# Kernel tuning notes

Hardware: AMD Instinct MI355X
Metric: run time of the kernel (lower is better)

Reference implementation:

```python
import jax, jax.numpy as jnp
import numpy as np

N_NODES = 50000
N_EDGES = 640000
D = 128  # input = hidden = output channels (must match for this module's forward to type-check)


def gcn_conv(x, W, b, src, dst, n):
    """PyG GCNConv: out = D^{-1/2} (A + I) D^{-1/2} (x @ W) + b.
    src = edge_index[0] (source/message sender), dst = edge_index[1] (target/aggregation index).
    """
    h = x @ W  # [n, d_out]
    loop = jnp.arange(n)
    s = jnp.concatenate([src, loop])  # add self-loops
    d = jnp.concatenate([dst, loop])
    deg = jax.ops.segment_sum(jnp.ones(s.shape[0], dtype=h.dtype), d, num_segments=n)
    dis = jax.lax.rsqrt(deg)  # deg >= 1 thanks to self-loops
    norm = dis[s] * dis[d]  # [E + n]
    msg = h[s] * norm[:, None]  # gather + scale (largest intermediate)
    return jax.ops.segment_sum(msg, d, num_segments=n) + b


def setup_inputs() -> dict:
    key = jax.random.key(0)
    ks = jax.random.split(key, 9)
    x = jax.random.normal(ks[0], (N_NODES, D), dtype=jnp.float32)
    edge_index_normal = jax.random.randint(ks[1], (2, N_EDGES), 0, N_NODES, dtype=jnp.int64 if jax.config.jax_enable_x64 else jnp.int32)
    edge_index_role = jax.random.randint(ks[2], (2, N_EDGES), 0, N_NODES, dtype=jnp.int64 if jax.config.jax_enable_x64 else jnp.int32)
    s = 1.0 / np.sqrt(D)
    W_role = jax.random.uniform(ks[3], (D, D), jnp.float32, -s, s)
    b_role = jnp.zeros((D,), jnp.float32)
    W2 = jax.random.uniform(ks[4], (D, D), jnp.float32, -s, s)
    b2 = jnp.zeros((D,), jnp.float32)
    W1 = jax.random.uniform(ks[5], (D, D), jnp.float32, -s, s)
    b1 = jnp.zeros((D,), jnp.float32)
    return {"x": x, "W_role": W_role, "b_role": b_role, "W2": W2, "b2": b2,
            "W1": W1, "b1": b1,
            "edge_index_normal": edge_index_normal, "edge_index_role": edge_index_role}


def reference(x, W_role, b_role, W2, b2, W1, b1, edge_index_normal, edge_index_role):
    n = x.shape[0]
    # conv_role on the role graph, then conv2 and conv1 on the normal graph.
    h = jax.nn.relu(gcn_conv(x, W_role, b_role, edge_index_role[0], edge_index_role[1], n))
    # dropout(p=0.5) is identity in eval mode
    h = jax.nn.relu(gcn_conv(h, W2, b2, edge_index_normal[0], edge_index_normal[1], n))
    out = gcn_conv(h, W1, b1, edge_index_normal[0], edge_index_normal[1], n)
    return out
```

## Files before the change

kernel.cpp:

```cpp
#include <hip/hip_runtime.h>
#include <hip/hip_fp16.h>

#define D 128
#define CHUNK 8192
#define BSH 7
#define BNODES 128
#define MAXNB 512
#define CAP 6144

__global__ __launch_bounds__(256) void p1_hist(const int* __restrict__ dst_n,
                                               const int* __restrict__ dst_r,
                                               int En, int Er,
                                               int* __restrict__ base2,
                                               int NB, int NC, int L) {
    int g = blockIdx.x / NC, c = blockIdx.x % NC;
    const int* dst = g ? dst_r : dst_n;
    int E = g ? Er : En;
    __shared__ int hist[MAXNB];
    for (int i = threadIdx.x; i < NB; i += 256) hist[i] = 0;
    __syncthreads();
    int e0 = c * CHUNK, e1 = min(e0 + CHUNK, E);
    for (int e = e0 + threadIdx.x; e < e1; e += 256)
        atomicAdd(&hist[dst[e] >> BSH], 1);
    __syncthreads();
    for (int b = threadIdx.x; b < NB; b += 256)
        base2[g * L + b * NC + c] = hist[b];
}

__global__ __launch_bounds__(1024) void scan_pass1(const int* __restrict__ data,
                                                   int* __restrict__ bsum2, int L, int nb) {
    int g = blockIdx.x / nb, b = blockIdx.x % nb;
    int i = b * 1024 + threadIdx.x;
    int v = (i < L) ? data[g * L + i] : 0;
    #pragma unroll
    for (int off = 32; off; off >>= 1) v += __shfl_down(v, off, 64);
    __shared__ int wsum[16];
    int lane = threadIdx.x & 63, wid = threadIdx.x >> 6;
    if (lane == 0) wsum[wid] = v;
    __syncthreads();
    if (threadIdx.x == 0) {
        int s = 0;
        for (int w = 0; w < 16; ++w) s += wsum[w];
        bsum2[g * 64 + b] = s;
    }
}

__global__ __launch_bounds__(128) void scan_pass2(int* __restrict__ bsum2, int nb) {
    int wid = threadIdx.x >> 6, lane = threadIdx.x & 63;
    int v = (lane < nb) ? bsum2[wid * 64 + lane] : 0;
    int incl = v;
    #pragma unroll
    for (int off = 1; off < 64; off <<= 1) {
        int t = __shfl_up(incl, off, 64);
        if (lane >= off) incl += t;
    }
    if (lane < nb) bsum2[wid * 64 + lane] = incl - v;
}

__global__ __launch_bounds__(1024) void scan_pass3(int* __restrict__ data,
                                                   const int* __restrict__ bsum2,
                                                   int L, int nb) {
    int g = blockIdx.x / nb, b = blockIdx.x % nb;
    int i = b * 1024 + threadIdx.x;
    int v = (i < L) ? data[g * L + i] : 0;
    int lane = threadIdx.x & 63, wid = threadIdx.x >> 6;
    int incl = v;
    #pragma unroll
    for (int off = 1; off < 64; off <<= 1) {
        int t = __shfl_up(incl, off, 64);
        if (lane >= off) incl += t;
    }
    __shared__ int wsum[16];
    if (lane == 63) wsum[wid] = incl;
    __syncthreads();
    if (threadIdx.x == 0) {
        int s = 0;
        for (int w = 0; w < 16; ++w) { int t = wsum[w]; wsum[w] = s; s += t; }
    }
    __syncthreads();
    if (i < L) data[g * L + i] = incl - v + wsum[wid] + bsum2[g * 64 + b];
}

__global__ __launch_bounds__(256) void p2_scatter(const int* __restrict__ src_n,
                                                  const int* __restrict__ dst_n,
                                                  const int* __restrict__ src_r,
                                                  const int* __restrict__ dst_r,
                                                  int En, int Er,
                                                  const int* __restrict__ base2,
                                                  unsigned int* __restrict__ part_n,
                                                  unsigned int* __restrict__ part_r,
                                                  int NB, int NC, int L) {
    int g = blockIdx.x / NC, c = blockIdx.x % NC;
    const int* src = g ? src_r : src_n;
    const int* dst = g ? dst_r : dst_n;
    unsigned int* part = g ? part_r : part_n;
    int E = g ? Er : En;
    __shared__ int cur[MAXNB];
    for (int b = threadIdx.x; b < NB; b += 256)
        cur[b] = base2[g * L + b * NC + c];
    __syncthreads();
    int e0 = c * CHUNK, e1 = min(e0 + CHUNK, E);
    for (int e = e0 + threadIdx.x; e < e1; e += 256) {
        int d = dst[e];
        int pos = atomicAdd(&cur[d >> BSH], 1);
        part[pos] = ((unsigned)d << 16) | (unsigned)src[e];
    }
}

__global__ __launch_bounds__(256) void p3_csr(const unsigned int* __restrict__ part_n,
                                              const unsigned int* __restrict__ part_r,
                                              const int* __restrict__ base2,
                                              int* __restrict__ rs2,
                                              float* __restrict__ dis2,
                                              unsigned short* __restrict__ csr_n,
                                              unsigned short* __restrict__ csr_r,
                                              int n, int NB, int NC, int L, int En, int Er) {
    int g = blockIdx.x / NB, b = blockIdx.x % NB;
    const unsigned int* part = g ? part_r : part_n;
    unsigned short* csr = g ? csr_r : csr_n;
    int E = g ? Er : En;
    __shared__ int deg[BNODES];
    __shared__ int cur[BNODES];
    __shared__ unsigned short buf[CAP];
    __shared__ int w0tot;
    int t = threadIdx.x;
    if (t < BNODES) deg[t] = 0;
    __syncthreads();
    int bstart = base2[g * L + b * NC];
    int bend = (b + 1 < NB) ? base2[g * L + (b + 1) * NC] : E;
    int sz = bend - bstart;
    for (int e = bstart + t; e < bend; e += 256)
        atomicAdd(&deg[(part[e] >> 16) & (BNODES - 1)], 1);
    __syncthreads();
    int incl = 0, v = 0;
    if (t < BNODES) {
        int lane = t & 63;
        v = deg[t];
        incl = v;
        #pragma unroll
        for (int off = 1; off < 64; off <<= 1) {
            int tt = __shfl_up(incl, off, 64);
            if (lane >= off) incl += tt;
        }
        if (t == 63) w0tot = incl;
    }
    __syncthreads();
    if (t < BNODES) {
        int excl = incl - v + ((t >= 64) ? w0tot : 0);
        cur[t] = excl;
        int idx = b * BNODES + t;
        if (idx < n) {
            rs2[g * (n + 1) + idx] = bstart + excl;
            dis2[g * n + idx] = rsqrtf((float)(deg[t] + 1));
        }
    }
    if (b == NB - 1 && t == 255) rs2[g * (n + 1) + n] = E;
    __syncthreads();
    if (sz <= CAP) {
        for (int e = bstart + t; e < bend; e += 256) {
            unsigned int p = part[e];
            int pos = atomicAdd(&cur[(p >> 16) & (BNODES - 1)], 1);
            buf[pos] = (unsigned short)(p & 0xffffu);
        }
        __syncthreads();
        for (int i = t; i < sz; i += 256) csr[bstart + i] = buf[i];
    } else {
        for (int e = bstart + t; e < bend; e += 256) {
            unsigned int p = part[e];
            int pos = atomicAdd(&cur[(p >> 16) & (BNODES - 1)], 1);
            csr[bstart + pos] = (unsigned short)(p & 0xffffu);
        }
    }
}


__global__ __launch_bounds__(256) void gemm_scale(const float* __restrict__ X,
                                                  const float* __restrict__ W,
                                                  const float* __restrict__ dis,
                                                  __half* __restrict__ Y, int n) {
    __shared__ float sX[128 * D];
    int t = threadIdx.x;
    int rg = t >> 4;
    int cg = (t & 15) << 3;
    int rb = blockIdx.x * 128;
    int rows = min(128, n - rb);

    float4* sX4 = (float4*)sX;
    for (int i = t; i < rows * 32; i += 256)
        sX4[i] = ((const float4*)X)[(size_t)rb * 32 + i];
    __syncthreads();

    float acc[8][8] = {};
    #pragma unroll 2
    for (int k0 = 0; k0 < D; k0 += 4) {
        float4 xr[8];
        #pragma unroll
        for (int r = 0; r < 8; ++r)
            xr[r] = *(const float4*)&sX[(rg * 8 + r) * D + k0];
        #pragma unroll
        for (int j = 0; j < 4; ++j) {
            float4 wa = *(const float4*)(W + (size_t)(k0 + j) * D + cg);
            float4 wb = *(const float4*)(W + (size_t)(k0 + j) * D + cg + 4);
            #pragma unroll
            for (int r = 0; r < 8; ++r) {
                float xv = ((const float*)&xr[r])[j];
                acc[r][0] += xv * wa.x; acc[r][1] += xv * wa.y;
                acc[r][2] += xv * wa.z; acc[r][3] += xv * wa.w;
                acc[r][4] += xv * wb.x; acc[r][5] += xv * wb.y;
                acc[r][6] += xv * wb.z; acc[r][7] += xv * wb.w;
            }
        }
    }
    #pragma unroll
    for (int r = 0; r < 8; ++r) {
        int row = rb + rg * 8 + r;
        if (row < n) {
            float dv = dis[row];
            __half2 p0 = __floats2half2_rn(acc[r][0] * dv, acc[r][1] * dv);
            __half2 p1 = __floats2half2_rn(acc[r][2] * dv, acc[r][3] * dv);
            __half2 p2 = __floats2half2_rn(acc[r][4] * dv, acc[r][5] * dv);
            __half2 p3 = __floats2half2_rn(acc[r][6] * dv, acc[r][7] * dv);
            uint4 o;
            o.x = *(unsigned*)&p0; o.y = *(unsigned*)&p1;
            o.z = *(unsigned*)&p2; o.w = *(unsigned*)&p3;
            *(uint4*)(Y + (size_t)row * D + cg) = o;
        }
    }
}

__global__ __launch_bounds__(256) void aggregate(const __half* __restrict__ g,
                                                 const int* __restrict__ rs,
                                                 const unsigned short* __restrict__ csr,
                                                 const float* __restrict__ dis,
                                                 const float* __restrict__ bias,
                                                 float* __restrict__ out, int n, int do_relu) {
    int v = blockIdx.x * 16 + (threadIdx.x >> 4);
    if (v >= n) return;
    int l16 = threadIdx.x & 15;
    const uint4* g4 = (const uint4*)g;
    float acc[8];
    {
        uint4 raw = g4[(size_t)v * 16 + l16];
        float2 f0 = __half22float2(*(__half2*)&raw.x);
        float2 f1 = __half22float2(*(__half2*)&raw.y);
        float2 f2 = __half22float2(*(__half2*)&raw.z);
        float2 f3 = __half22float2(*(__half2*)&raw.w);
        acc[0] = f0.x; acc[1] = f0.y; acc[2] = f1.x; acc[3] = f1.y;
        acc[4] = f2.x; acc[5] = f2.y; acc[6] = f3.x; acc[7] = f3.y;
    }
    int e = rs[v], end = rs[v + 1];
    while (e < end) {
        int m = min(16, end - e);
        int sid = (e + l16 < end) ? (int)csr[e + l16] : 0;
        int j = 0;
        for (; j + 7 < m; j += 8) {
            uint4 raw[8];
            #pragma unroll
            for (int u = 0; u < 8; ++u) {
                int s = __shfl(sid, j + u, 16);
                raw[u] = g4[(size_t)s * 16 + l16];
            }
            #pragma unroll
            for (int u = 0; u < 8; ++u) {
                float2 f0 = __half22float2(*(__half2*)&raw[u].x);
                float2 f1 = __half22float2(*(__half2*)&raw[u].y);
                float2 f2 = __half22float2(*(__half2*)&raw[u].z);
                float2 f3 = __half22float2(*(__half2*)&raw[u].w);
                acc[0] += f0.x; acc[1] += f0.y; acc[2] += f1.x; acc[3] += f1.y;
                acc[4] += f2.x; acc[5] += f2.y; acc[6] += f3.x; acc[7] += f3.y;
            }
        }
        for (; j + 3 < m; j += 4) {
            uint4 raw[4];
            #pragma unroll
            for (int u = 0; u < 4; ++u) {
                int s = __shfl(sid, j + u, 16);
                raw[u] = g4[(size_t)s * 16 + l16];
            }
            #pragma unroll
            for (int u = 0; u < 4; ++u) {
                float2 f0 = __half22float2(*(__half2*)&raw[u].x);
                float2 f1 = __half22float2(*(__half2*)&raw[u].y);
                float2 f2 = __half22float2(*(__half2*)&raw[u].z);
                float2 f3 = __half22float2(*(__half2*)&raw[u].w);
                acc[0] += f0.x; acc[1] += f0.y; acc[2] += f1.x; acc[3] += f1.y;
                acc[4] += f2.x; acc[5] += f2.y; acc[6] += f3.x; acc[7] += f3.y;
            }
        }
        for (; j < m; ++j) {
            int s = __shfl(sid, j, 16);
            uint4 raw = g4[(size_t)s * 16 + l16];
            float2 f0 = __half22float2(*(__half2*)&raw.x);
            float2 f1 = __half22float2(*(__half2*)&raw.y);
            float2 f2 = __half22float2(*(__half2*)&raw.z);
            float2 f3 = __half22float2(*(__half2*)&raw.w);
            acc[0] += f0.x; acc[1] += f0.y; acc[2] += f1.x; acc[3] += f1.y;
            acc[4] += f2.x; acc[5] += f2.y; acc[6] += f3.x; acc[7] += f3.y;
        }
        e += m;
    }
    float dv = dis[v];
    const float4* b4 = (const float4*)bias;
    float4 ba = b4[2 * l16], bb = b4[2 * l16 + 1];
    float4 o0, o1;
    o0.x = dv * acc[0] + ba.x; o0.y = dv * acc[1] + ba.y;
    o0.z = dv * acc[2] + ba.z; o0.w = dv * acc[3] + ba.w;
    o1.x = dv * acc[4] + bb.x; o1.y = dv * acc[5] + bb.y;
    o1.z = dv * acc[6] + bb.z; o1.w = dv * acc[7] + bb.w;
    if (do_relu) {
        o0.x = fmaxf(o0.x, 0.f); o0.y = fmaxf(o0.y, 0.f);
        o0.z = fmaxf(o0.z, 0.f); o0.w = fmaxf(o0.w, 0.f);
        o1.x = fmaxf(o1.x, 0.f); o1.y = fmaxf(o1.y, 0.f);
        o1.z = fmaxf(o1.z, 0.f); o1.w = fmaxf(o1.w, 0.f);
    }
    float4* orow = (float4*)(out + (size_t)v * D);
    orow[2 * l16] = o0;
    orow[2 * l16 + 1] = o1;
}


extern "C" void kernel_launch(void* const* d_in, const int* in_sizes, int n_in,
                              void* d_out, int out_size, void* d_ws, size_t ws_size,
                              hipStream_t stream) {
    const float* x      = (const float*)d_in[0];
    const float* W_role = (const float*)d_in[1];
    const float* b_role = (const float*)d_in[2];
    const float* W2     = (const float*)d_in[3];
    const float* b2     = (const float*)d_in[4];
    const float* W1     = (const float*)d_in[5];
    const float* b1     = (const float*)d_in[6];
    const int*   ein    = (const int*)d_in[7];
    const int*   eir    = (const int*)d_in[8];

    int n  = in_sizes[0] / D;
    int En = in_sizes[7] / 2;
    int Er = in_sizes[8] / 2;
    const int* src_n = ein;
    const int* dst_n = ein + En;
    const int* src_r = eir;
    const int* dst_r = eir + Er;
    float* out = (float*)d_out;

    int NB = (n + BNODES - 1) >> BSH;
    int Emax = En > Er ? En : Er;
    int NC = (Emax + CHUNK - 1) / CHUNK;
    int L  = NB * NC;
    int nb_scan = (L + 1023) / 1024;

    char* p = (char*)d_ws;
    auto alloc = [&](size_t bytes) { char* r = p; p += (bytes + 255) & ~(size_t)255; return r; };
    __half*         gbuf   = (__half*)alloc((size_t)n * D * sizeof(__half));
    float*          dis2   = (float*)alloc((size_t)2 * n * sizeof(float));
    int*            rs2    = (int*)alloc((size_t)2 * (n + 1) * sizeof(int));
    int*            base2  = (int*)alloc((size_t)2 * L * sizeof(int));
    int*            bsum2  = (int*)alloc(512);
    unsigned int*   part_n = (unsigned int*)alloc((size_t)En * sizeof(unsigned int));
    unsigned int*   part_r = (unsigned int*)alloc((size_t)Er * sizeof(unsigned int));
    unsigned short* csr    = (unsigned short*)alloc((size_t)(En + Er) * sizeof(unsigned short));
    float* dis_n = dis2;
    float* dis_r = dis2 + n;
    int*   rs_n  = rs2;
    int*   rs_r  = rs2 + (n + 1);
    unsigned short* csr_n = csr;
    unsigned short* csr_r = csr + En;

    p1_hist<<<2 * NC, 256, 0, stream>>>(dst_n, dst_r, En, Er, base2, NB, NC, L);
    scan_pass1<<<2 * nb_scan, 1024, 0, stream>>>(base2, bsum2, L, nb_scan);
    scan_pass2<<<1, 128, 0, stream>>>(bsum2, nb_scan);
    scan_pass3<<<2 * nb_scan, 1024, 0, stream>>>(base2, bsum2, L, nb_scan);
    p2_scatter<<<2 * NC, 256, 0, stream>>>(src_n, dst_n, src_r, dst_r, En, Er,
                                           base2, part_n, part_r, NB, NC, L);
    p3_csr<<<2 * NB, 256, 0, stream>>>(part_n, part_r, base2, rs2, dis2,
                                       csr_n, csr_r, n, NB, NC, L, En, Er);

    int gblk = (n + 127) / 128;
    int ablk = (n + 15) / 16;
    gemm_scale<<<gblk, 256, 0, stream>>>(x, W_role, dis_r, gbuf, n);
    aggregate<<<ablk, 256, 0, stream>>>(gbuf, rs_r, csr_r, dis_r, b_role, out, n, 1);
    gemm_scale<<<gblk, 256, 0, stream>>>(out, W2, dis_n, gbuf, n);
    aggregate<<<ablk, 256, 0, stream>>>(gbuf, rs_n, csr_n, dis_n, b2, out, n, 1);
    gemm_scale<<<gblk, 256, 0, stream>>>(out, W1, dis_n, gbuf, n);
    aggregate<<<ablk, 256, 0, stream>>>(gbuf, rs_n, csr_n, dis_n, b1, out, n, 0);
}
```

Before: 299.4 us.

## Use fp16 MFMA GEMM for hidden layers with half-precision intermediate activations

Replaces the fp32 scalar GEMM for the second and third layers with a kernel built on the fp16 MFMA 16x16x32 instruction. Weights are transposed to fp16 by a small prep kernel. The aggregate kernel now writes hidden activations as fp16 instead of fp32, which halves that traffic and feeds the MFMA GEMM directly. The cost is lower precision in the intermediate activations and an extra launch for the weight conversion. The MFMA epilogue also uses scalar 2-byte stores, which may coalesce poorly.

```diff
diff --git a/kernel.cpp b/kernel.cpp
--- a/kernel.cpp
+++ b/kernel.cpp
@@ -7,6 +7,10 @@
 #define BNODES 128
 #define MAXNB 512
 #define CAP 6144
+#define PADK 136
+
+typedef _Float16 half8 __attribute__((ext_vector_type(8)));
+typedef float float4v __attribute__((ext_vector_type(4)));
 
 __global__ __launch_bounds__(256) void p1_hist(const int* __restrict__ dst_n,
                                                const int* __restrict__ dst_r,
@@ -173,6 +177,19 @@
     }
 }
 
+__global__ __launch_bounds__(256) void wprep(const float* __restrict__ W2,
+                                             const float* __restrict__ W1,
+                                             _Float16* __restrict__ Wt2,
+                                             _Float16* __restrict__ Wt1) {
+    int i = blockIdx.x * 256 + threadIdx.x;
+    int m = i >> 14;
+    int idx = i & 16383;
+    int nn = idx >> 7, k = idx & 127;
+    const float* W = m ? W1 : W2;
+    _Float16* Wt = m ? Wt1 : Wt2;
+    Wt[nn * 128 + k] = (_Float16)W[k * 128 + nn];
+}
+
 
 __global__ __launch_bounds__(256) void gemm_scale(const float* __restrict__ X,
                                                   const float* __restrict__ W,
@@ -228,12 +245,75 @@
     }
 }
 
+__global__ __launch_bounds__(256) void gemm_mfma(const _Float16* __restrict__ Xh,
+                                                 const _Float16* __restrict__ Wt,
+                                                 const float* __restrict__ dis,
+                                                 _Float16* __restrict__ Y, int n) {
+    __shared__ _Float16 sA[128 * PADK];
+    __shared__ _Float16 sB[128 * PADK];
+    int t = threadIdx.x;
+    int rb = blockIdx.x * 128;
+    int rows = min(128, n - rb);
+
+    for (int i = t; i < 128 * 16; i += 256) {
+        int r = i >> 4, s = i & 15;
+        *(uint4*)&sB[r * PADK + s * 8] = ((const uint4*)Wt)[i];
+    }
+    for (int i = t; i < rows * 16; i += 256) {
+        int r = i >> 4, s = i & 15;
+        *(uint4*)&sA[r * PADK + s * 8] = ((const uint4*)(Xh + (size_t)rb * D))[i];
+    }
+    if (rows < 128) {
+        for (int i = rows * 16 + t; i < 128 * 16; i += 256) {
+            int r = i >> 4, s = i & 15;
+            *(uint4*)&sA[r * PADK + s * 8] = make_uint4(0, 0, 0, 0);
+        }
+    }
+    __syncthreads();
+
+    int w = t >> 6, lane = t & 63;
+    int quad = lane >> 4, l16 = lane & 15;
+    float4v acc[2][8];
+    #pragma unroll
+    for (int rt = 0; rt < 2; ++rt)
+        #pragma unroll
+        for (int ct = 0; ct < 8; ++ct)
+            acc[rt][ct] = (float4v){0.f, 0.f, 0.f, 0.f};
+
+    #pragma unroll
+    for (int k0 = 0; k0 < 128; k0 += 32) {
+        half8 a0 = *(half8*)&sA[(w * 32 + l16) * PADK + k0 + quad * 8];
+        half8 a1 = *(half8*)&sA[(w * 32 + 16 + l16) * PADK + k0 + quad * 8];
+        #pragma unroll
+        for (int ct = 0; ct < 8; ++ct) {
+            half8 b = *(half8*)&sB[(ct * 16 + l16) * PADK + k0 + quad * 8];
+            acc[0][ct] = __builtin_amdgcn_mfma_f32_16x16x32_f16(a0, b, acc[0][ct], 0, 0, 0);
+            acc[1][ct] = __builtin_amdgcn_mfma_f32_16x16x32_f16(a1, b, acc[1][ct], 0, 0, 0);
+        }
+    }
+    #pragma unroll
+    for (int rt = 0; rt < 2; ++rt) {
+        #pragma unroll
+        for (int r = 0; r < 4; ++r) {
+            int row = rb + w * 32 + rt * 16 + quad * 4 + r;
+            if (row < n) {
+                float dv = dis[row];
+                #pragma unroll
+                for (int ct = 0; ct < 8; ++ct)
+                    Y[(size_t)row * D + ct * 16 + l16] = (_Float16)(acc[rt][ct][r] * dv);
+            }
+        }
+    }
+}
+
 __global__ __launch_bounds__(256) void aggregate(const __half* __restrict__ g,
                                                  const int* __restrict__ rs,
                                                  const unsigned short* __restrict__ csr,
                                                  const float* __restrict__ dis,
                                                  const float* __restrict__ bias,
-                                                 float* __restrict__ out, int n, int do_relu) {
+                                                 float* __restrict__ outf,
+                                                 _Float16* __restrict__ outh,
+                                                 int n, int do_relu, int write_half) {
     int v = blockIdx.x * 16 + (threadIdx.x >> 4);
     if (v >= n) return;
     int l16 = threadIdx.x & 15;
@@ -302,20 +382,29 @@
     float dv = dis[v];
     const float4* b4 = (const float4*)bias;
     float4 ba = b4[2 * l16], bb = b4[2 * l16 + 1];
-    float4 o0, o1;
-    o0.x = dv * acc[0] + ba.x; o0.y = dv * acc[1] + ba.y;
-    o0.z = dv * acc[2] + ba.z; o0.w = dv * acc[3] + ba.w;
-    o1.x = dv * acc[4] + bb.x; o1.y = dv * acc[5] + bb.y;
-    o1.z = dv * acc[6] + bb.z; o1.w = dv * acc[7] + bb.w;
+    float o[8];
+    o[0] = dv * acc[0] + ba.x; o[1] = dv * acc[1] + ba.y;
+    o[2] = dv * acc[2] + ba.z; o[3] = dv * acc[3] + ba.w;
+    o[4] = dv * acc[4] + bb.x; o[5] = dv * acc[5] + bb.y;
+    o[6] = dv * acc[6] + bb.z; o[7] = dv * acc[7] + bb.w;
     if (do_relu) {
-        o0.x = fmaxf(o0.x, 0.f); o0.y = fmaxf(o0.y, 0.f);
-        o0.z = fmaxf(o0.z, 0.f); o0.w = fmaxf(o0.w, 0.f);
-        o1.x = fmaxf(o1.x, 0.f); o1.y = fmaxf(o1.y, 0.f);
-        o1.z = fmaxf(o1.z, 0.f); o1.w = fmaxf(o1.w, 0.f);
-    }
-    float4* orow = (float4*)(out + (size_t)v * D);
-    orow[2 * l16] = o0;
-    orow[2 * l16 + 1] = o1;
+        #pragma unroll
+        for (int i = 0; i < 8; ++i) o[i] = fmaxf(o[i], 0.f);
+    }
+    if (write_half) {
+        __half2 p0 = __floats2half2_rn(o[0], o[1]);
+        __half2 p1 = __floats2half2_rn(o[2], o[3]);
+        __half2 p2 = __floats2half2_rn(o[4], o[5]);
+        __half2 p3 = __floats2half2_rn(o[6], o[7]);
+        uint4 pk;
+        pk.x = *(unsigned*)&p0; pk.y = *(unsigned*)&p1;
+        pk.z = *(unsigned*)&p2; pk.w = *(unsigned*)&p3;
+        ((uint4*)outh)[(size_t)v * 16 + l16] = pk;
+    } else {
+        float4* orow = (float4*)(outf + (size_t)v * D);
+        orow[2 * l16] = make_float4(o[0], o[1], o[2], o[3]);
+        orow[2 * l16 + 1] = make_float4(o[4], o[5], o[6], o[7]);
+    }
 }
 
 
@@ -350,6 +439,9 @@
     char* p = (char*)d_ws;
     auto alloc = [&](size_t bytes) { char* r = p; p += (bytes + 255) & ~(size_t)255; return r; };
     __half*         gbuf   = (__half*)alloc((size_t)n * D * sizeof(__half));
+    _Float16*       hbuf   = (_Float16*)alloc((size_t)n * D * sizeof(_Float16));
+    _Float16*       Wt2    = (_Float16*)alloc((size_t)D * D * sizeof(_Float16));
+    _Float16*       Wt1    = (_Float16*)alloc((size_t)D * D * sizeof(_Float16));
     float*          dis2   = (float*)alloc((size_t)2 * n * sizeof(float));
     int*            rs2    = (int*)alloc((size_t)2 * (n + 1) * sizeof(int));
     int*            base2  = (int*)alloc((size_t)2 * L * sizeof(int));
@@ -372,13 +464,17 @@
                                            base2, part_n, part_r, NB, NC, L);
     p3_csr<<<2 * NB, 256, 0, stream>>>(part_n, part_r, base2, rs2, dis2,
                                        csr_n, csr_r, n, NB, NC, L, En, Er);
+    wprep<<<128, 256, 0, stream>>>(W2, W1, Wt2, Wt1);
 
     int gblk = (n + 127) / 128;
     int ablk = (n + 15) / 16;
     gemm_scale<<<gblk, 256, 0, stream>>>(x, W_role, dis_r, gbuf, n);
-    aggregate<<<ablk, 256, 0, stream>>>(gbuf, rs_r, csr_r, dis_r, b_role, out, n, 1);
-    gemm_scale<<<gblk, 256, 0, stream>>>(out, W2, dis_n, gbuf, n);
-    aggregate<<<ablk, 256, 0, stream>>>(gbuf, rs_n, csr_n, dis_n, b2, out, n, 1);
-    gemm_scale<<<gblk, 256, 0, stream>>>(out, W1, dis_n, gbuf, n);
-    aggregate<<<ablk, 256, 0, stream>>>(gbuf, rs_n, csr_n, dis_n, b1, out, n, 0);
-}
+    aggregate<<<ablk, 256, 0, stream>>>(gbuf, rs_r, csr_r, dis_r, b_role,
+                                        nullptr, hbuf, n, 1, 1);
+    gemm_mfma<<<gblk, 256, 0, stream>>>(hbuf, Wt2, dis_n, (_Float16*)gbuf, n);
+    aggregate<<<ablk, 256, 0, stream>>>(gbuf, rs_n, csr_n, dis_n, b2,
+                                        nullptr, hbuf, n, 1, 1);
+    gemm_mfma<<<gblk, 256, 0, stream>>>(hbuf, Wt1, dis_n, (_Float16*)gbuf, n);
+    aggregate<<<ablk, 256, 0, stream>>>(gbuf, rs_n, csr_n, dis_n, b1,
+                                        out, nullptr, n, 0, 0);
+}
```

New measurement: 270.0 us. 9.8% less time.
